# Kernel tuning notes

Hardware: AMD Instinct MI355X
Metric: run time of the kernel (lower is better)

The kernel has to match this reference:

```python
import jax, jax.numpy as jnp
import numpy as np

H, R, B, T = 512, 4, 16, 4096

def _glorot(key, shape):
    return jax.random.uniform(key, shape, minval=-1.0, maxval=1.0) * jnp.sqrt(2.0 / sum(shape))

def setup_inputs() -> dict:
    key = jax.random.key(0)
    k1, k2, k3, k4, k5 = jax.random.split(key, 5)
    return {
        "x_seq": jax.random.normal(k5, (B, T, H), dtype=jnp.float32),
        "a_diag": _glorot(k1, (H,)).astype(jnp.float32),
        "p_vec": _glorot(k2, (H, R)).astype(jnp.float32),
        "q_vec": _glorot(k3, (H, R)).astype(jnp.float32),
        "b_mat": _glorot(k4, (H, H)).astype(jnp.float32),
    }

def reference(x_seq, a_diag, p_vec, q_vec, b_mat):
    # A = diag(a_diag) + P Q^T  (DPLR structure, materialized as in the source)
    A = jnp.diag(a_diag) + p_vec @ q_vec.T            # [H, H]
    # Precompute B @ x_t for all timesteps/batches: bx[b,t,k] = sum_h b_mat[k,h] x[b,t,h]
    bx = jnp.einsum("bth,kh->btk", x_seq, b_mat)      # [B, T, H]
    h0 = jnp.zeros((x_seq.shape[0], a_diag.shape[0]), dtype=x_seq.dtype)  # [B, H]

    def step(h, bx_t):
        # h_{t} = A h_{t-1} + B x_t, batched: (h @ A^T)
        h = h @ A.T + bx_t
        return h, h

    _, h_seq = jax.lax.scan(step, h0, jnp.swapaxes(bx, 0, 1))  # [T, B, H]
    return jnp.swapaxes(h_seq, 0, 1)                            # [B, T, H]
```

## Files before the change

kernel.cpp:

```cpp
#include <hip/hip_runtime.h>
#include <hip/hip_bf16.h>

#define H 512
#define RNK 4
#define BATCH 16
#define TT 4096
#define MTOT (BATCH * TT)

#define BM 128
#define BN 128
#define BK 64

#define NCHUNK 128
#define JWARM 32

#define LDK 72

typedef __attribute__((ext_vector_type(8))) short bf16x8;
typedef __attribute__((ext_vector_type(4))) float f32x4;

__device__ inline unsigned short f2bf(float f) {
    unsigned u = __float_as_uint(f);
    u += 0x7FFFu + ((u >> 16) & 1u);
    return (unsigned short)(u >> 16);
}
__device__ inline float bflo(unsigned w) { return __uint_as_float(w << 16); }
__device__ inline float bfhi(unsigned w) { return __uint_as_float(w & 0xFFFF0000u); }
__device__ inline float rfl(float x) {
    return __uint_as_float(__builtin_amdgcn_readfirstlane(__float_as_uint(x)));
}

__global__ __launch_bounds__(256) void convert_kernel(
    const float* __restrict__ src, unsigned short* __restrict__ dst, int n4)
{
    int i = blockIdx.x * blockDim.x + threadIdx.x;
    const int stride = gridDim.x * blockDim.x;
    for (; i < n4; i += stride) {
        float4 v = ((const float4*)src)[i];
        ushort4 o = { f2bf(v.x), f2bf(v.y), f2bf(v.z), f2bf(v.w) };
        ((ushort4*)dst)[i] = o;
    }
}

__global__ __launch_bounds__(256, 2) void gemm_x32_kernel(
    const float* __restrict__ X, const unsigned short* __restrict__ Wbf,
    unsigned short* __restrict__ C)
{
    __shared__ unsigned short As[BM * BK];
    __shared__ unsigned short Bs[BN * BK];
    const int l = blockIdx.x;
    const int t = (l & 7) * ((MTOT / BM) * (H / BN) / 8) + (l >> 3);
    const size_t mbase = (size_t)(t >> 2) * BM;
    const int nbase = (t & 3) * BN;

    const int tid  = threadIdx.x;
    const int lane = tid & 63;
    const int wave = tid >> 6;
    const int wm = (wave >> 1) * 64;
    const int wn = (wave & 1) * 64;
    const int r  = lane & 15;
    const int qd = lane >> 4;
    const float* Xb = X + mbase * H;
    const unsigned short* Wb = Wbf + (size_t)nbase * H;

    f32x4 acc[4][4];
    #pragma unroll
    for (int i = 0; i < 4; ++i)
        #pragma unroll
        for (int j = 0; j < 4; ++j)
            acc[i][j] = (f32x4){0.f, 0.f, 0.f, 0.f};

    float4 ra[8];
    auto loadRA = [&](int kt) {
        const int k0 = kt * BK;
        #pragma unroll
        for (int i = 0; i < 8; ++i) {
            const int idx = tid + i * 256;
            const int row = idx >> 4;
            const int c4  = (idx & 15) * 4;
            ra[i] = *(const float4*)(Xb + (size_t)row * H + k0 + c4);
        }
    };
    auto issueW = [&](int kt) {
        const int k0 = kt * BK;
        #pragma unroll
        for (int s = 0; s < 4; ++s) {
            const int seg = wave * 4 + s;
            const int off  = seg * 1024 + lane * 16;
            const int row  = off >> 7;
            const int slot = ((off >> 4) & 7) ^ (row & 7);
            const unsigned short* gb = Wb + (size_t)row * H + k0 + slot * 8;
            __builtin_amdgcn_global_load_lds(
                (const __attribute__((address_space(1))) unsigned int*)gb,
                (__attribute__((address_space(3))) unsigned int*)&Bs[seg * 512], 16, 0, 0);
        }
    };

    issueW(0);
    loadRA(0);

    const int nt = H / BK;
    for (int kt = 0; kt < nt; ++kt) {
        #pragma unroll
        for (int i = 0; i < 8; ++i) {
            const int idx = tid + i * 256;
            const int row = idx >> 4;
            const int c4  = (idx & 15) * 4;
            const float4 v = ra[i];
            ushort4 wa = { f2bf(v.x), f2bf(v.y), f2bf(v.z), f2bf(v.w) };
            const int el = (row * BK + c4) ^ ((row & 7) << 3);
            *(ushort4*)&As[el] = wa;
        }
        __syncthreads();
        if (kt + 1 < nt) loadRA(kt + 1);
        #pragma unroll
        for (int kk = 0; kk < BK; kk += 32) {
            bf16x8 af[4], bfr[4];
            #pragma unroll
            for (int i = 0; i < 4; ++i) {
                const int arow = wm + i * 16 + r;
                af[i] = *(const bf16x8*)&As[(arow * BK + kk + qd * 8) ^ ((arow & 7) << 3)];
            }
            #pragma unroll
            for (int j = 0; j < 4; ++j) {
                const int brow = wn + j * 16 + r;
                bfr[j] = *(const bf16x8*)&Bs[(brow * BK + kk + qd * 8) ^ ((brow & 7) << 3)];
            }
            #pragma unroll
            for (int i = 0; i < 4; ++i)
                #pragma unroll
                for (int j = 0; j < 4; ++j)
                    acc[i][j] = __builtin_amdgcn_mfma_f32_16x16x32_bf16(
                        af[i], bfr[j], acc[i][j], 0, 0, 0);
        }
        __syncthreads();
        if (kt + 1 < nt) issueW(kt + 1);
    }

    #pragma unroll
    for (int i = 0; i < 4; ++i)
        #pragma unroll
        for (int j = 0; j < 4; ++j)
            #pragma unroll
            for (int e = 0; e < 4; ++e) {
                const size_t m = mbase + wm + i * 16 + qd * 4 + e;
                const int n = nbase + wn + j * 16 + r;
                C[m * H + n] = f2bf(acc[i][j][e]);
            }
}

__global__ __launch_bounds__(64) void scan_bf_kernel(
    const unsigned short* __restrict__ bx, float* __restrict__ out,
    const float* __restrict__ a_diag, const float* __restrict__ p_vec,
    const float* __restrict__ q_vec, int nchunk, int warm_max)
{
    const int lane = threadIdx.x;
    const int c = blockIdx.x;
    const int b = blockIdx.y;
    const int L = TT / nchunk;
    const int d0 = lane * 8;

    float ak[8], g[8];
    float4 pk[8], qk[8];
    #pragma unroll
    for (int j = 0; j < 8; ++j) {
        ak[j] = a_diag[d0 + j];
        pk[j] = *(const float4*)(p_vec + (d0 + j) * RNK);
        qk[j] = *(const float4*)(q_vec + (d0 + j) * RNK);
        g[j] = 0.f;
    }

    float Gx[3][4][4];
    {
        float part[3][16];
        #pragma unroll
        for (int k = 0; k < 3; ++k)
            #pragma unroll
            for (int v = 0; v < 16; ++v) part[k][v] = 0.f;
        #pragma unroll
        for (int d = 0; d < 8; ++d) {
            const float a1 = ak[d], a2 = a1 * a1;
            const float qr[4] = {qk[d].x, qk[d].y, qk[d].z, qk[d].w};
            const float pc[4] = {pk[d].x, pk[d].y, pk[d].z, pk[d].w};
            #pragma unroll
            for (int r = 0; r < 4; ++r)
                #pragma unroll
                for (int cc = 0; cc < 4; ++cc) {
                    const float qp = qr[r] * pc[cc];
                    part[0][r * 4 + cc] += qp;
                    part[1][r * 4 + cc] += qp * a1;
                    part[2][r * 4 + cc] += qp * a2;
                }
        }
        #pragma unroll
        for (int off = 32; off > 0; off >>= 1)
            #pragma unroll
            for (int k = 0; k < 3; ++k)
                #pragma unroll
                for (int v = 0; v < 16; ++v)
                    part[k][v] += __shfl_xor(part[k][v], off);
        #pragma unroll
        for (int k = 0; k < 3; ++k)
            #pragma unroll
            for (int r = 0; r < 4; ++r)
                #pragma unroll
                for (int cc = 0; cc < 4; ++cc)
                    Gx[k][r][cc] = rfl(part[k][r * 4 + cc]);
    }

    const int warm  = (c == 0) ? 0 : warm_max;
    const int steps = warm + L;
    const int nb    = steps >> 2;
    const int tstart = c * L - warm;
    const unsigned short* src = bx + (size_t)b * TT * H + d0;
    float* dst = out + (size_t)b * TT * H + d0;

    uint4 ring[4];
    #pragma unroll
    for (int j = 0; j < 4; ++j)
        ring[j] = *(const uint4*)(src + (size_t)(tstart + j) * H);

    for (int blk = 0; blk < nb; ++blk) {
        const int i0 = blk * 4;
        float yp[4][4];
        float gs[4][8];

        #pragma unroll
        for (int j = 0; j < 4; ++j) {
            float y0 = 0.f, y1 = 0.f, y2 = 0.f, y3 = 0.f;
            #pragma unroll
            for (int d = 0; d < 8; ++d) {
                y0 += qk[d].x * g[d]; y1 += qk[d].y * g[d];
                y2 += qk[d].z * g[d]; y3 += qk[d].w * g[d];
            }
            yp[j][0] = y0; yp[j][1] = y1; yp[j][2] = y2; yp[j][3] = y3;

            const uint4 cur = ring[j];
            int iload = i0 + 4 + j;
            if (iload > steps - 1) iload = steps - 1;
            ring[j] = *(const uint4*)(src + (size_t)(tstart + iload) * H);

            float u[8];
            u[0] = bflo(cur.x); u[1] = bfhi(cur.x);
            u[2] = bflo(cur.y); u[3] = bfhi(cur.y);
            u[4] = bflo(cur.z); u[5] = bfhi(cur.z);
            u[6] = bflo(cur.w); u[7] = bfhi(cur.w);
            #pragma unroll
            for (int d = 0; d < 8; ++d) { g[d] = ak[d] * g[d] + u[d]; gs[j][d] = g[d]; }
        }

        #pragma unroll
        for (int off = 32; off > 0; off >>= 1)
            #pragma unroll
            for (int j = 0; j < 4; ++j)
                #pragma unroll
                for (int r = 0; r < 4; ++r)
                    yp[j][r] += __shfl_xor(yp[j][r], off);

        float sv[4][4];
        #pragma unroll
        for (int r = 0; r < 4; ++r) sv[0][r] = yp[0][r];
        #pragma unroll
        for (int r = 0; r < 4; ++r) {
            float t = yp[1][r];
            #pragma unroll
            for (int cc = 0; cc < 4; ++cc) t += Gx[0][r][cc] * sv[0][cc];
            sv[1][r] = t;
        }
        #pragma unroll
        for (int r = 0; r < 4; ++r) {
            float t = yp[2][r];
            #pragma unroll
            for (int cc = 0; cc < 4; ++cc) t += Gx[1][r][cc] * sv[0][cc];
            #pragma unroll
            for (int cc = 0; cc < 4; ++cc) t += Gx[0][r][cc] * sv[1][cc];
            sv[2][r] = t;
        }
        #pragma unroll
        for (int r = 0; r < 4; ++r) {
            float t = yp[3][r];
            #pragma unroll
            for (int cc = 0; cc < 4; ++cc) t += Gx[2][r][cc] * sv[0][cc];
            #pragma unroll
            for (int cc = 0; cc < 4; ++cc) t += Gx[1][r][cc] * sv[1][cc];
            #pragma unroll
            for (int cc = 0; cc < 4; ++cc) t += Gx[0][r][cc] * sv[2][cc];
            sv[3][r] = t;
        }

        const bool dostore = (i0 >= warm);
        float e[8];
        #pragma unroll
        for (int d = 0; d < 8; ++d) e[d] = 0.f;
        #pragma unroll
        for (int j = 0; j < 4; ++j) {
            #pragma unroll
            for (int d = 0; d < 8; ++d) {
                const float ps = pk[d].x * sv[j][0] + pk[d].y * sv[j][1]
                               + pk[d].z * sv[j][2] + pk[d].w * sv[j][3];
                e[d] = ak[d] * e[d] + ps;
            }
            if (dostore) {
                float* dd = dst + (size_t)(tstart + i0 + j) * H;
                *(float4*)dd       = (float4){gs[j][0] + e[0], gs[j][1] + e[1],
                                              gs[j][2] + e[2], gs[j][3] + e[3]};
                *(float4*)(dd + 4) = (float4){gs[j][4] + e[4], gs[j][5] + e[5],
                                              gs[j][6] + e[6], gs[j][7] + e[7]};
            }
        }
        #pragma unroll
        for (int d = 0; d < 8; ++d) g[d] = gs[3][d] + e[d];
    }
}

__global__ __launch_bounds__(256) void gemm_fused_kernel(
    const float* __restrict__ X, const float* __restrict__ W, float* __restrict__ bx)
{
    __shared__ unsigned short As[BM * LDK];
    __shared__ unsigned short Bs[BN * LDK];
    const int tid  = threadIdx.x;
    const int lane = tid & 63;
    const int wave = tid >> 6;
    const int wm = (wave >> 1) * 64;
    const int wn = (wave & 1) * 64;
    const size_t mbase = (size_t)blockIdx.x * BM;
    const int nbase = blockIdx.y * BN;
    const float* Xb = X + mbase * H;
    const float* Wb = W + (size_t)nbase * H;
    f32x4 acc[4][4];
    #pragma unroll
    for (int i = 0; i < 4; ++i)
        #pragma unroll
        for (int j = 0; j < 4; ++j)
            acc[i][j] = (f32x4){0.f, 0.f, 0.f, 0.f};
    const int r  = lane & 15;
    const int qd = lane >> 4;
    for (int k0 = 0; k0 < H; k0 += BK) {
        #pragma unroll
        for (int i = 0; i < 8; ++i) {
            int idx = tid + i * 256;
            int row = idx >> 4;
            int c4  = (idx & 15) * 4;
            float4 va = *(const float4*)(Xb + (size_t)row * H + k0 + c4);
            float4 vb = *(const float4*)(Wb + (size_t)row * H + k0 + c4);
            ushort4 wa = { f2bf(va.x), f2bf(va.y), f2bf(va.z), f2bf(va.w) };
            ushort4 wb = { f2bf(vb.x), f2bf(vb.y), f2bf(vb.z), f2bf(vb.w) };
            *(ushort4*)&As[row * LDK + c4] = wa;
            *(ushort4*)&Bs[row * LDK + c4] = wb;
        }
        __syncthreads();
        #pragma unroll
        for (int kk = 0; kk < BK; kk += 32) {
            bf16x8 af[4], bfr[4];
            #pragma unroll
            for (int i = 0; i < 4; ++i)
                af[i] = *(const bf16x8*)&As[(wm + i * 16 + r) * LDK + kk + qd * 8];
            #pragma unroll
            for (int j = 0; j < 4; ++j)
                bfr[j] = *(const bf16x8*)&Bs[(wn + j * 16 + r) * LDK + kk + qd * 8];
            #pragma unroll
            for (int i = 0; i < 4; ++i)
                #pragma unroll
                for (int j = 0; j < 4; ++j)
                    acc[i][j] = __builtin_amdgcn_mfma_f32_16x16x32_bf16(
                        af[i], bfr[j], acc[i][j], 0, 0, 0);
        }
        __syncthreads();
    }
    #pragma unroll
    for (int i = 0; i < 4; ++i)
        #pragma unroll
        for (int j = 0; j < 4; ++j)
            #pragma unroll
            for (int e = 0; e < 4; ++e) {
                int m = wm + i * 16 + qd * 4 + e;
                int n = wn + j * 16 + r;
                bx[(mbase + m) * H + nbase + n] = acc[i][j][e];
            }
}

__global__ __launch_bounds__(64) void scan_f32_kernel(
    const float* __restrict__ bx, float* __restrict__ out,
    const float* __restrict__ a_diag, const float* __restrict__ p_vec,
    const float* __restrict__ q_vec)
{
    const int lane = threadIdx.x;
    const int b = blockIdx.y;
    const int d0 = lane * 8;
    float ak[8], hk[8];
    float4 pk[8], qk[8];
    #pragma unroll
    for (int j = 0; j < 8; ++j) {
        ak[j] = a_diag[d0 + j];
        pk[j] = *(const float4*)(p_vec + (d0 + j) * RNK);
        qk[j] = *(const float4*)(q_vec + (d0 + j) * RNK);
        hk[j] = 0.f;
    }
    const float* src = bx + (size_t)b * TT * H + d0;
    float* dst = out + (size_t)b * TT * H + d0;
    for (int i = 0; i < TT; ++i) {
        const float* sp = src + (size_t)i * H;
        float4 va = *(const float4*)sp, vb = *(const float4*)(sp + 4);
        float u[8] = {va.x, va.y, va.z, va.w, vb.x, vb.y, vb.z, vb.w};
        float s0 = 0.f, s1 = 0.f, s2 = 0.f, s3 = 0.f;
        #pragma unroll
        for (int j = 0; j < 8; ++j) {
            s0 += qk[j].x * hk[j]; s1 += qk[j].y * hk[j];
            s2 += qk[j].z * hk[j]; s3 += qk[j].w * hk[j];
        }
        #pragma unroll
        for (int off = 32; off > 0; off >>= 1) {
            s0 += __shfl_xor(s0, off); s1 += __shfl_xor(s1, off);
            s2 += __shfl_xor(s2, off); s3 += __shfl_xor(s3, off);
        }
        #pragma unroll
        for (int j = 0; j < 8; ++j)
            hk[j] = ak[j] * hk[j] + (pk[j].x * s0 + pk[j].y * s1 + pk[j].z * s2 + pk[j].w * s3) + u[j];
        float* d = dst + (size_t)i * H;
        *(float4*)d = (float4){hk[0], hk[1], hk[2], hk[3]};
        *(float4*)(d + 4) = (float4){hk[4], hk[5], hk[6], hk[7]};
    }
}

extern "C" void kernel_launch(void* const* d_in, const int* in_sizes, int n_in,
                              void* d_out, int out_size, void* d_ws, size_t ws_size,
                              hipStream_t stream) {
    (void)in_sizes; (void)n_in; (void)out_size;
    const float* x = (const float*)d_in[0];
    const float* a = (const float*)d_in[1];
    const float* p = (const float*)d_in[2];
    const float* q = (const float*)d_in[3];
    const float* w = (const float*)d_in[4];
    float* out = (float*)d_out;

    const size_t nx    = (size_t)MTOT * H;
    const size_t wbf_b = (size_t)H * H * 2;
    const size_t bxb_b = nx * 2;

    if (d_ws != nullptr && ws_size >= wbf_b + bxb_b) {
        unsigned short* wbf  = (unsigned short*)d_ws;
        unsigned short* bxbf = wbf + (size_t)H * H;
        convert_kernel<<<256, 256, 0, stream>>>(w, wbf, (int)(H * H / 4));
        gemm_x32_kernel<<<(MTOT / BM) * (H / BN), 256, 0, stream>>>(x, wbf, bxbf);
        dim3 g2(NCHUNK, BATCH), b2(64);
        scan_bf_kernel<<<g2, b2, 0, stream>>>(bxbf, out, a, p, q, NCHUNK, JWARM);
    } else {
        dim3 g1(MTOT / BM, H / BN), b1(256);
        gemm_fused_kernel<<<g1, b1, 0, stream>>>(x, w, out);
        dim3 g2(1, BATCH), b2(64);
        scan_f32_kernel<<<g2, b2, 0, stream>>>(out, out, a, p, q);
    }
}
```

Baseline: 319.4 us.

## Double-buffer LDS tiles in bf16 GEMM to drop one barrier per k-step

The input-projection GEMM now uses two LDS buffers for both A and B tiles. The next W tile is issued asynchronously into the alternate buffer right after the barrier, which removes the second __syncthreads per iteration and overlaps global-to-LDS loads with MFMA work. Explicit vmcnt/lgkmcnt waits and a raw s_barrier replace the implicit sync, and LDS use doubles, which may reduce occupancy. Correctness relies on the hand-counted vmcnt(8) matching the outstanding load order.

```diff
diff --git a/kernel.cpp b/kernel.cpp
--- a/kernel.cpp
+++ b/kernel.cpp
@@ -46,8 +46,8 @@
     const float* __restrict__ X, const unsigned short* __restrict__ Wbf,
     unsigned short* __restrict__ C)
 {
-    __shared__ unsigned short As[BM * BK];
-    __shared__ unsigned short Bs[BN * BK];
+    __shared__ unsigned short As[2][BM * BK];
+    __shared__ unsigned short Bs[2][BN * BK];
     const int l = blockIdx.x;
     const int t = (l & 7) * ((MTOT / BM) * (H / BN) / 8) + (l >> 3);
     const size_t mbase = (size_t)(t >> 2) * BM;
@@ -81,7 +81,7 @@
             ra[i] = *(const float4*)(Xb + (size_t)row * H + k0 + c4);
         }
     };
-    auto issueW = [&](int kt) {
+    auto issueW = [&](int kt, int p) {
         const int k0 = kt * BK;
         #pragma unroll
         for (int s = 0; s < 4; ++s) {
@@ -92,15 +92,16 @@
             const unsigned short* gb = Wb + (size_t)row * H + k0 + slot * 8;
             __builtin_amdgcn_global_load_lds(
                 (const __attribute__((address_space(1))) unsigned int*)gb,
-                (__attribute__((address_space(3))) unsigned int*)&Bs[seg * 512], 16, 0, 0);
+                (__attribute__((address_space(3))) unsigned int*)&Bs[p][seg * 512], 16, 0, 0);
         }
     };
 
-    issueW(0);
     loadRA(0);
+    issueW(0, 0);
 
     const int nt = H / BK;
     for (int kt = 0; kt < nt; ++kt) {
+        const int p = kt & 1;
         #pragma unroll
         for (int i = 0; i < 8; ++i) {
             const int idx = tid + i * 256;
@@ -109,22 +110,30 @@
             const float4 v = ra[i];
             ushort4 wa = { f2bf(v.x), f2bf(v.y), f2bf(v.z), f2bf(v.w) };
             const int el = (row * BK + c4) ^ ((row & 7) << 3);
-            *(ushort4*)&As[el] = wa;
-        }
-        __syncthreads();
-        if (kt + 1 < nt) loadRA(kt + 1);
+            *(ushort4*)&As[p][el] = wa;
+        }
+        if (kt + 1 < nt) {
+            loadRA(kt + 1);
+            asm volatile("s_waitcnt vmcnt(8)" ::: "memory");
+        } else {
+            asm volatile("s_waitcnt vmcnt(0)" ::: "memory");
+        }
+        asm volatile("s_waitcnt lgkmcnt(0)" ::: "memory");
+        __builtin_amdgcn_s_barrier();
+        __builtin_amdgcn_sched_barrier(0);
+        if (kt + 1 < nt) issueW(kt + 1, p ^ 1);
         #pragma unroll
         for (int kk = 0; kk < BK; kk += 32) {
             bf16x8 af[4], bfr[4];
             #pragma unroll
             for (int i = 0; i < 4; ++i) {
                 const int arow = wm + i * 16 + r;
-                af[i] = *(const bf16x8*)&As[(arow * BK + kk + qd * 8) ^ ((arow & 7) << 3)];
+                af[i] = *(const bf16x8*)&As[p][(arow * BK + kk + qd * 8) ^ ((arow & 7) << 3)];
             }
             #pragma unroll
             for (int j = 0; j < 4; ++j) {
                 const int brow = wn + j * 16 + r;
-                bfr[j] = *(const bf16x8*)&Bs[(brow * BK + kk + qd * 8) ^ ((brow & 7) << 3)];
+                bfr[j] = *(const bf16x8*)&Bs[p][(brow * BK + kk + qd * 8) ^ ((brow & 7) << 3)];
             }
             #pragma unroll
             for (int i = 0; i < 4; ++i)
@@ -133,8 +142,6 @@
                     acc[i][j] = __builtin_amdgcn_mfma_f32_16x16x32_bf16(
                         af[i], bfr[j], acc[i][j], 0, 0, 0);
         }
-        __syncthreads();
-        if (kt + 1 < nt) issueW(kt + 1);
     }
 
     #pragma unroll
```

After: 322.2 us. Within noise of the previous version (+0.9%).
